# Kernel tuning notes

Measured on AMD Instinct MI355X. Metric: run time of the kernel, lower is better.

## Reference

```python
import jax, jax.numpy as jnp
import numpy as np

L, B, T, C, H, FC = 8, 4, 2048, 1024, 16, 4
HD = C // H  # head dim = 64
DFF = FC * C  # 4096


def _layernorm(x, g, b, eps=1e-5):
    mu = jnp.mean(x, axis=-1, keepdims=True)
    var = jnp.mean(jnp.square(x - mu), axis=-1, keepdims=True)
    return (x - mu) * jax.lax.rsqrt(var + eps) * g + b


def setup_inputs() -> dict:
    key = jax.random.key(0)
    ks = jax.random.split(key, 18)
    s = 0.02
    d = {}
    d["x"] = jax.random.normal(ks[0], (B, T, C), jnp.float32)
    d["ln1_g"] = jnp.ones((L, C), jnp.float32)
    d["ln1_b"] = jnp.zeros((L, C), jnp.float32)
    d["ln2_g"] = jnp.ones((L, C), jnp.float32)
    d["ln2_b"] = jnp.zeros((L, C), jnp.float32)
    d["wq"] = jax.random.normal(ks[1], (L, C, C), jnp.float32) * s
    d["bq"] = jnp.zeros((L, C), jnp.float32)
    d["wk"] = jax.random.normal(ks[2], (L, C, C), jnp.float32) * s
    d["bk"] = jnp.zeros((L, C), jnp.float32)
    d["wv"] = jax.random.normal(ks[3], (L, C, C), jnp.float32) * s
    d["bv"] = jnp.zeros((L, C), jnp.float32)
    d["wo"] = jax.random.normal(ks[4], (L, C, C), jnp.float32) * s
    d["bo"] = jnp.zeros((L, C), jnp.float32)
    d["w1"] = jax.random.normal(ks[5], (L, C, DFF), jnp.float32) * s
    d["b1"] = jnp.zeros((L, DFF), jnp.float32)
    d["w2"] = jax.random.normal(ks[6], (L, DFF, C), jnp.float32) * s
    d["b2"] = jnp.zeros((L, C), jnp.float32)
    return d


def _forward(x, ln1_g, ln1_b, ln2_g, ln2_b, wq, bq, wk, bk, wv, bv, wo, bo, w1, b1, w2, b2):
    mask = jnp.tril(jnp.ones((T, T), dtype=bool))  # causal mask (block_size buffer)
    scale = 1.0 / np.sqrt(HD).astype(np.float32)

    def block(h, p):
        g1, be1, g2, be2, Wq, Bq, Wk, Bk, Wv, Bv, Wo, Bo, W1, B1, W2, B2 = p
        hn = _layernorm(h, g1, be1)
        # heads: [B, H, T, HD]
        q = (hn @ Wq + Bq).reshape(B, T, H, HD).transpose(0, 2, 1, 3)
        k = (hn @ Wk + Bk).reshape(B, T, H, HD).transpose(0, 2, 1, 3)
        v = (hn @ Wv + Bv).reshape(B, T, H, HD).transpose(0, 2, 1, 3)
        att = jnp.einsum('bhid,bhjd->bhij', q, k) * scale
        att = jnp.where(mask, att, -jnp.inf)
        att = jax.nn.softmax(att, axis=-1)
        y = jnp.einsum('bhij,bhjd->bhid', att, v)
        y = y.transpose(0, 2, 1, 3).reshape(B, T, C) @ Wo + Bo
        h = h + y
        m = _layernorm(h, g2, be2)
        h = h + jax.nn.gelu(m @ W1 + B1, approximate=False) @ W2 + B2
        return h, None

    params = (ln1_g, ln1_b, ln2_g, ln2_b, wq, bq, wk, bk, wv, bv, wo, bo, w1, b1, w2, b2)
    x, _ = jax.lax.scan(block, x, params)
    return x


def reference(x, ln1_g, ln1_b, ln2_g, ln2_b, wq, bq, wk, bk, wv, bv, wo, bo, w1, b1, w2, b2):
    return _forward(x, ln1_g, ln1_b, ln2_g, ln2_b, wq, bq, wk, bk, wv, bv, wo, bo, w1, b1, w2, b2)
```

## Files before the change

### kernel.cpp

```cpp
#include <hip/hip_runtime.h>
#include <hip/hip_bf16.h>

#define LL 8
#define BBx 4
#define TT 2048
#define CC 1024
#define HH 16
#define HDD 64
#define DFFx 4096
#define MMx 8192

typedef __bf16 bf16;
typedef __attribute__((ext_vector_type(8))) __bf16 bf16x8;
typedef __attribute__((ext_vector_type(4))) __bf16 bf16x4;
typedef __attribute__((ext_vector_type(4))) float f32x4;
typedef __attribute__((ext_vector_type(8))) unsigned short u16x8;

#define QSCALE 0.18033688f

__device__ __forceinline__ unsigned short bfbits(float v) {
  return __builtin_bit_cast(unsigned short, (__bf16)v);
}

__device__ __forceinline__ float fexp2(float x) {
#if __has_builtin(__builtin_amdgcn_exp2f)
  return __builtin_amdgcn_exp2f(x);
#else
  float r;
  asm volatile("v_exp_f32 %0, %1\n\ts_nop 0" : "=v"(r) : "v"(x));
  return r;
#endif
}

__device__ __forceinline__ int xcd_swz(int id, int nwg) {
  return (id & 7) * (nwg >> 3) + (id >> 3);
}

#define GLDS(gp, lp) __builtin_amdgcn_global_load_lds( \
    (const __attribute__((address_space(1))) void*)(gp), \
    (__attribute__((address_space(3))) void*)(lp), 16, 0, 0)

__global__ __launch_bounds__(256) void transpose_cast(
    const float* __restrict__ W, bf16* __restrict__ Wt,
    int K, int N, long srcStride, long dstStride)
{
  __shared__ float tile[32][33];
  const float* Wl = W + (size_t)blockIdx.z * srcStride;
  bf16* Wtl = Wt + (size_t)blockIdx.z * dstStride;
  const int n0 = blockIdx.x * 32, k0 = blockIdx.y * 32;
  const int tx = threadIdx.x, ty = threadIdx.y;
#pragma unroll
  for (int i = 0; i < 32; i += 8)
    tile[ty + i][tx] = Wl[(size_t)(k0 + ty + i) * N + n0 + tx];
  __syncthreads();
#pragma unroll
  for (int i = 0; i < 32; i += 8)
    Wtl[(size_t)(n0 + ty + i) * K + k0 + tx] = (bf16)tile[tx][ty + i];
}

__global__ __launch_bounds__(256) void ln_cmb(
    float* __restrict__ h, const float* __restrict__ p0, const float* __restrict__ p1,
    const float* __restrict__ gamma, const float* __restrict__ beta,
    bf16* __restrict__ out)
{
  const int row = blockIdx.x, tid = threadIdx.x;
  const size_t base = (size_t)row * CC + tid * 4;
  float4 v = *(const float4*)(h + base);
  if (p0) {
    const float4 a = *(const float4*)(p0 + base);
    const float4 b = *(const float4*)(p1 + base);
    v.x += a.x + b.x; v.y += a.y + b.y; v.z += a.z + b.z; v.w += a.w + b.w;
    *(float4*)(h + base) = v;
  }
  if (!out) return;
  float s  = v.x + v.y + v.z + v.w;
  float ss = v.x * v.x + v.y * v.y + v.z * v.z + v.w * v.w;
#pragma unroll
  for (int o = 32; o >= 1; o >>= 1) {
    s  += __shfl_xor(s, o);
    ss += __shfl_xor(ss, o);
  }
  __shared__ float rs[4], rss[4];
  const int w = tid >> 6, l = tid & 63;
  if (l == 0) { rs[w] = s; rss[w] = ss; }
  __syncthreads();
  s  = rs[0] + rs[1] + rs[2] + rs[3];
  ss = rss[0] + rss[1] + rss[2] + rss[3];
  const float mu = s * (1.f / CC);
  const float rstd = rsqrtf(ss * (1.f / CC) - mu * mu + 1e-5f);
  const float4 g  = *(const float4*)(gamma + tid * 4);
  const float4 be = *(const float4*)(beta + tid * 4);
  bf16x4 o4;
  o4[0] = (bf16)((v.x - mu) * rstd * g.x + be.x);
  o4[1] = (bf16)((v.y - mu) * rstd * g.y + be.y);
  o4[2] = (bf16)((v.z - mu) * rstd * g.z + be.z);
  o4[3] = (bf16)((v.w - mu) * rstd * g.w + be.w);
  *(bf16x4*)(out + (size_t)row * CC + tid * 4) = o4;
}

template<int EPI>
__global__ __launch_bounds__(256, 4) void gemm128(
    const bf16* __restrict__ A, const bf16* __restrict__ Bt,
    const float* __restrict__ bias0,
    float* __restrict__ p0, float* __restrict__ p1,
    int M, int N, int K, int lda)
{
  __shared__ __align__(16) bf16 sA[128 * 64];
  __shared__ __align__(16) bf16 sB[128 * 64];
  const int nx = N >> 7;
  int wk = xcd_swz((int)blockIdx.x, (int)gridDim.x);
  int koff = 0;
  float* part = p0;
  bool addb = true;
  if constexpr (EPI == 1) {
    const int tiles = nx * (M >> 7);
    const int ks = wk / tiles;
    wk -= ks * tiles;
    koff = ks * K;
    addb = (ks == 0);
    part = ks ? p1 : p0;
  }
  const int m0 = (wk / nx) * 128;
  const int n0 = (wk % nx) * 128;
  const int tid = threadIdx.x;
  const int w = tid >> 6, l = tid & 63;
  const int wr = w >> 1, wc = w & 1;
  const int lr = l & 15, lk = l >> 4;

  f32x4 acc[4][4] = {};
  const int NT = K >> 6;

  for (int kt = 0; kt < NT; ++kt) {
#pragma unroll
    for (int i = 0; i < 4; ++i) {
      const int e = (tid << 4) + (i << 12);
      const int ro = e >> 7, co = (e & 127) >> 1;
      GLDS(A + (size_t)(m0 + ro) * lda + kt * 64 + koff + co, sA + (e >> 1));
      GLDS(Bt + (size_t)(n0 + ro) * lda + kt * 64 + koff + co, sB + (e >> 1));
    }
    __syncthreads();
#pragma unroll
    for (int kk = 0; kk < 2; ++kk) {
      bf16x8 af[4], bfr[4];
#pragma unroll
      for (int i = 0; i < 4; ++i)
        af[i] = *(const bf16x8*)&sA[(wr * 64 + i * 16 + lr) * 64 + kk * 32 + lk * 8];
#pragma unroll
      for (int j = 0; j < 4; ++j)
        bfr[j] = *(const bf16x8*)&sB[(wc * 64 + j * 16 + lr) * 64 + kk * 32 + lk * 8];
#pragma unroll
      for (int i = 0; i < 4; ++i)
#pragma unroll
        for (int j = 0; j < 4; ++j)
          acc[i][j] = __builtin_amdgcn_mfma_f32_16x16x32_bf16(af[i], bfr[j], acc[i][j], 0, 0, 0);
    }
    __syncthreads();
  }
  float bv4[4];
#pragma unroll
  for (int j = 0; j < 4; ++j)
    bv4[j] = addb ? bias0[n0 + wc * 64 + j * 16 + lr] : 0.f;
#pragma unroll
  for (int i = 0; i < 4; ++i) {
    const int mrow = m0 + wr * 64 + i * 16 + lk * 4;
#pragma unroll
    for (int r = 0; r < 4; ++r) {
      float* rowp = part + (size_t)(mrow + r) * N + n0 + wc * 64;
#pragma unroll
      for (int j = 0; j < 4; ++j)
        rowp[j * 16 + lr] = acc[i][j][r] + bv4[j];
    }
  }
  (void)M;
}

template<int EPI>
__global__ __launch_bounds__(512, 2) void gemm256(
    const bf16* __restrict__ A, const bf16* __restrict__ Bt,
    const float* __restrict__ bias0, const float* __restrict__ bias1,
    const float* __restrict__ bias2,
    bf16* __restrict__ o0, bf16* __restrict__ o1, bf16* __restrict__ o2,
    float* __restrict__ p0w, float* __restrict__ p1w,
    int M, int N, int K, int lda)
{
  __shared__ __align__(16) bf16 sA[2][256 * 64];
  __shared__ __align__(16) bf16 sB[2][256 * 64];
  const int nx = N >> 8;
  int wk = xcd_swz((int)blockIdx.x, (int)gridDim.x);
  int koff = 0;
  float* part = p0w;
  bool addb = true;
  if constexpr (EPI == 1) {
    const int tiles = nx * (M >> 8);
    const int ks = wk / tiles;
    wk -= ks * tiles;
    koff = ks * K;
    addb = (ks == 0);
    part = ks ? p1w : p0w;
  }
  const int m0 = (wk / nx) * 256;
  const int n0 = (wk % nx) * 256;
  const int tid = threadIdx.x;
  const int w = tid >> 6, l = tid & 63;
  const int wm = w >> 2, wn = w & 3;
  const int lr = l & 15, lk = l >> 4;
  const int sr = tid >> 3, ss = tid & 7;
  const int gcs = (ss ^ (sr & 7)) << 3;

  f32x4 acc[8][4] = {};
  const int NT = K >> 6;

  auto stageq = [&](int b, int kt, int q) {
    const int gc = gcs + kt * 64 + koff;
    const int rb = (q & 1) * 128;
    if (q < 2) {
#pragma unroll
      for (int i = 0; i < 2; ++i) {
        const int r = rb + sr + i * 64;
        GLDS(A + (size_t)(m0 + r) * lda + gc, &sA[b][r * 64 + ss * 8]);
      }
    } else {
#pragma unroll
      for (int i = 0; i < 2; ++i) {
        const int r = rb + sr + i * 64;
        GLDS(Bt + (size_t)(n0 + r) * lda + gc, &sB[b][r * 64 + ss * 8]);
      }
    }
  };

  stageq(0, 0, 0); stageq(0, 0, 1); stageq(0, 0, 2); stageq(0, 0, 3);
  asm volatile("s_waitcnt vmcnt(2)" ::: "memory");
  __builtin_amdgcn_s_barrier();

  bf16x8 af[8], bf2[2];
  for (int t = 0; t < NT; ++t) {
    const int cur = t & 1, nxt = cur ^ 1;
    const bool pre = (t + 1 < NT);
#pragma unroll
    for (int ph = 0; ph < 4; ++ph) {
      const int kk = ph >> 1, nh = ph & 1;
      if (nh == 0) {
#pragma unroll
        for (int m = 0; m < 8; ++m) {
          const int row = wm * 128 + m * 16 + lr;
          af[m] = *(const bf16x8*)&sA[cur][row * 64 + (((kk * 4 + lk) ^ (row & 7)) << 3)];
        }
      }
#pragma unroll
      for (int j2 = 0; j2 < 2; ++j2) {
        const int row = nh * 128 + wn * 32 + j2 * 16 + lr;
        bf2[j2] = *(const bf16x8*)&sB[cur][row * 64 + (((kk * 4 + lk) ^ (row & 7)) << 3)];
      }
      if (pre) stageq(nxt, t + 1, ph);
      if (ph == 0 || ph == 3) {
        if (pre) asm volatile("s_waitcnt vmcnt(2)" ::: "memory");
        else     asm volatile("s_waitcnt vmcnt(0)" ::: "memory");
      }
      __builtin_amdgcn_s_barrier();
      asm volatile("s_waitcnt lgkmcnt(0)" ::: "memory");
      __builtin_amdgcn_sched_barrier(0);
      __builtin_amdgcn_s_setprio(1);
#pragma unroll
      for (int m = 0; m < 8; ++m)
#pragma unroll
        for (int j2 = 0; j2 < 2; ++j2)
          acc[m][nh * 2 + j2] = __builtin_amdgcn_mfma_f32_16x16x32_bf16(
              af[m], bf2[j2], acc[m][nh * 2 + j2], 0, 0, 0);
      __builtin_amdgcn_s_setprio(0);
      __builtin_amdgcn_s_barrier();
    }
  }

  if constexpr (EPI == 0) {
    const int seg = n0 >> 10;
    const float* bp = (seg == 0) ? bias0 : (seg == 1 ? bias1 : bias2);
    if (seg < 2) {
      const float qs = (seg == 0) ? QSCALE : 1.0f;
      float bv4[4];
      int hh4[4], dd4[4];
#pragma unroll
      for (int jj = 0; jj < 4; ++jj) {
        const int c1024 = (n0 + (jj >> 1) * 128 + wn * 32 + (jj & 1) * 16 + lr) & 1023;
        bv4[jj] = bp[c1024];
        hh4[jj] = c1024 >> 6;
        dd4[jj] = c1024 & 63;
      }
      bf16* dst = (seg == 0) ? o0 : o1;
#pragma unroll
      for (int m = 0; m < 8; ++m) {
        const int mrow = m0 + wm * 128 + m * 16 + lk * 4;
        const int bidx = mrow >> 11, t = mrow & 2047;
#pragma unroll
        for (int r = 0; r < 4; ++r) {
#pragma unroll
          for (int jj = 0; jj < 4; ++jj)
            dst[(((size_t)(bidx * HH + hh4[jj])) * TT + t + r) * HDD + dd4[jj]] =
                (bf16)((acc[m][jj][r] + bv4[jj]) * qs);
        }
      }
    } else {
      char* scb = (char*)((w < 4) ? (&sA[0][0] + w * 8192) : (&sB[0][0] + (w - 4) * 8192));
#pragma unroll
      for (int jj = 0; jj < 4; ++jj) {
        const int dloc = (jj >> 1) * 32 + (jj & 1) * 16 + lr;
        const int dglob = (n0 & 1023) + (jj >> 1) * 128 + wn * 32 + (jj & 1) * 16 + lr;
        const float bv = bias2[dglob];
#pragma unroll
        for (int m = 0; m < 8; ++m) {
          ushort4 pk;
          pk.x = bfbits(acc[m][jj][0] + bv);
          pk.y = bfbits(acc[m][jj][1] + bv);
          pk.z = bfbits(acc[m][jj][2] + bv);
          pk.w = bfbits(acc[m][jj][3] + bv);
          *(ushort4*)(scb + dloc * 256 + (((m * 16 + lk * 4) * 2) ^ ((dloc & 7) << 4))) = pk;
        }
      }
      asm volatile("s_waitcnt lgkmcnt(0)" ::: "memory");
      const int bidx = m0 >> 11;
      const int tb = (m0 & 2047) + wm * 128;
      const int c = l & 15;
#pragma unroll
      for (int g = 0; g < 16; ++g) {
        const int dloc = g * 4 + lk;
        const int dglob = (n0 & 1023) + (dloc >> 5) * 128 + wn * 32 + (dloc & 31);
        const int hh = dglob >> 6, dd = dglob & 63;
        u16x8 val = *(const u16x8*)(scb + dloc * 256 + ((c * 16) ^ ((dloc & 7) << 4)));
        *(u16x8*)&o2[(((size_t)(bidx * HH + hh)) * HDD + dd) * TT + tb + c * 8] = val;
      }
    }
  } else if constexpr (EPI == 1) {
    float bv4[4];
#pragma unroll
    for (int jj = 0; jj < 4; ++jj)
      bv4[jj] = addb ? bias0[n0 + (jj >> 1) * 128 + wn * 32 + (jj & 1) * 16 + lr] : 0.f;
#pragma unroll
    for (int m = 0; m < 8; ++m) {
      const int mrow = m0 + wm * 128 + m * 16 + lk * 4;
#pragma unroll
      for (int r = 0; r < 4; ++r) {
        float* rowp = part + (size_t)(mrow + r) * N + n0 + wn * 32;
        rowp[lr]        = acc[m][0][r] + bv4[0];
        rowp[16 + lr]   = acc[m][1][r] + bv4[1];
        rowp[128 + lr]  = acc[m][2][r] + bv4[2];
        rowp[144 + lr]  = acc[m][3][r] + bv4[3];
      }
    }
  } else {
    float bv4[4];
#pragma unroll
    for (int jj = 0; jj < 4; ++jj)
      bv4[jj] = bias0[n0 + (jj >> 1) * 128 + wn * 32 + (jj & 1) * 16 + lr];
#pragma unroll
    for (int m = 0; m < 8; ++m) {
      const int mrow = m0 + wm * 128 + m * 16 + lk * 4;
#pragma unroll
      for (int r = 0; r < 4; ++r) {
        bf16* rowp = o0 + (size_t)(mrow + r) * N + n0 + wn * 32;
        const float x0 = acc[m][0][r] + bv4[0];
        const float x1 = acc[m][1][r] + bv4[1];
        const float x2 = acc[m][2][r] + bv4[2];
        const float x3 = acc[m][3][r] + bv4[3];
        rowp[lr]       = (bf16)(0.5f * x0 * (1.f + erff(x0 * 0.70710678f)));
        rowp[16 + lr]  = (bf16)(0.5f * x1 * (1.f + erff(x1 * 0.70710678f)));
        rowp[128 + lr] = (bf16)(0.5f * x2 * (1.f + erff(x2 * 0.70710678f)));
        rowp[144 + lr] = (bf16)(0.5f * x3 * (1.f + erff(x3 * 0.70710678f)));
      }
    }
  }
  (void)M;
}

__global__ __launch_bounds__(256) void attn_fwd(
    const bf16* __restrict__ Q, const bf16* __restrict__ Kk,
    const bf16* __restrict__ Vt, bf16* __restrict__ O)
{
  const int wk = xcd_swz((int)blockIdx.x, (int)gridDim.x);
  const int bh = wk >> 3;
  const int xt = wk & 7;
  const int tid = threadIdx.x;
  const int w = tid >> 6, l = tid & 63;
  const int lr = l & 15, lk = l >> 4;
  const int bidx = bh >> 4, hh = bh & 15;

  const bf16* Qp = Q  + (size_t)bh * (TT * HDD);
  const bf16* Kp = Kk + (size_t)bh * (TT * HDD);
  const bf16* Vp = Vt + (size_t)bh * (HDD * TT);

  __shared__ __align__(16) bf16 sK[64 * 64];
  __shared__ __align__(16) bf16 sV[64 * 64];
  __shared__ __align__(16) bf16 sP[4][16 * 64];
  bf16* sPw = &sP[w][0];

  const int swz = (lr & 7) * 8;
  const int srow = tid >> 3;
  const int scol = (((tid & 7) ^ (srow & 7)) << 3);
  const int sdst = tid << 3;

  for (int half = 0; half < 2; ++half) {
    const int qtile = (half == 0) ? xt : (15 - xt);
    const int q0 = qtile * 128;

    bf16x8 qf[2][2];
#pragma unroll
    for (int qi = 0; qi < 2; ++qi)
#pragma unroll
      for (int dk = 0; dk < 2; ++dk)
        qf[qi][dk] = *(const bf16x8*)&Qp[(size_t)(q0 + w * 32 + qi * 16 + lr) * HDD + dk * 32 + lk * 8];

    f32x4 accO[2][4] = {};
    float mrun[2] = {-__builtin_inff(), -__builtin_inff()};
    float lrun[2] = {0.f, 0.f};
    const int wqmax = q0 + w * 32 + 31;
    const int kvend = q0 + 128;

    for (int kv = 0; kv < kvend; kv += 64) {
      __syncthreads();
#pragma unroll
      for (int i = 0; i < 2; ++i) {
        GLDS(Kp + (size_t)(kv + srow + i * 32) * HDD + scol, sK + sdst + i * 2048);
        GLDS(Vp + (size_t)(srow + i * 32) * TT + kv + scol, sV + sdst + i * 2048);
      }
      __syncthreads();

      if (kv <= wqmax) {
#pragma unroll
        for (int qi = 0; qi < 2; ++qi) {
          f32x4 st[4];
#pragma unroll
          for (int kt = 0; kt < 4; ++kt) {
            f32x4 z = {0.f, 0.f, 0.f, 0.f};
#pragma unroll
            for (int dk = 0; dk < 2; ++dk) {
              bf16x8 kf = *(const bf16x8*)&sK[(kt * 16 + lr) * 64 + ((dk * 32 + lk * 8) ^ swz)];
              z = __builtin_amdgcn_mfma_f32_16x16x32_bf16(kf, qf[qi][dk], z, 0, 0, 0);
            }
            st[kt] = z;
          }
          const int qabs_base = q0 + w * 32 + qi * 16;
          float pm = -__builtin_inff();
          if (kv + 63 > qabs_base) {
            const int qabs = qabs_base + lr;
#pragma unroll
            for (int kt = 0; kt < 4; ++kt)
#pragma unroll
              for (int r = 0; r < 4; ++r) {
                const int kvabs = kv + kt * 16 + lk * 4 + r;
                float val = (kvabs > qabs) ? -__builtin_inff() : st[kt][r];
                st[kt][r] = val;
                pm = fmaxf(pm, val);
              }
          } else {
#pragma unroll
            for (int kt = 0; kt < 4; ++kt)
#pragma unroll
              for (int r = 0; r < 4; ++r) pm = fmaxf(pm, st[kt][r]);
          }
          pm = fmaxf(pm, __shfl_xor(pm, 16));
          pm = fmaxf(pm, __shfl_xor(pm, 32));
          const float mnew = fmaxf(mrun[qi], pm);
          const float alpha = fexp2(mrun[qi] - mnew);
          mrun[qi] = mnew;
          float psum = 0.f;
#pragma unroll
          for (int kt = 0; kt < 4; ++kt) {
            const float p0v = fexp2(st[kt][0] - mnew);
            const float p1v = fexp2(st[kt][1] - mnew);
            const float p2v = fexp2(st[kt][2] - mnew);
            const float p3v = fexp2(st[kt][3] - mnew);
            psum += p0v + p1v + p2v + p3v;
            ushort4 pk;
            pk.x = bfbits(p0v); pk.y = bfbits(p1v); pk.z = bfbits(p2v); pk.w = bfbits(p3v);
            *(ushort4*)&sPw[lr * 64 + ((kt * 16 + lk * 4) ^ swz)] = pk;
          }
          psum += __shfl_xor(psum, 16);
          psum += __shfl_xor(psum, 32);
          lrun[qi] = lrun[qi] * alpha + psum;
          f32x4 al4;
#pragma unroll
          for (int r = 0; r < 4; ++r) al4[r] = __shfl(alpha, lk * 4 + r);
#pragma unroll
          for (int dj = 0; dj < 4; ++dj) accO[qi][dj] *= al4;
#pragma unroll
          for (int kt2 = 0; kt2 < 2; ++kt2) {
            bf16x8 pf = *(const bf16x8*)&sPw[lr * 64 + ((kt2 * 32 + lk * 8) ^ swz)];
#pragma unroll
            for (int dj = 0; dj < 4; ++dj) {
              bf16x8 vf = *(const bf16x8*)&sV[(dj * 16 + lr) * 64 + ((kt2 * 32 + lk * 8) ^ swz)];
              accO[qi][dj] = __builtin_amdgcn_mfma_f32_16x16x32_bf16(pf, vf, accO[qi][dj], 0, 0, 0);
            }
          }
        }
      }
    }

#pragma unroll
    for (int qi = 0; qi < 2; ++qi) {
      const float linv = 1.f / lrun[qi];
      f32x4 li4;
#pragma unroll
      for (int r = 0; r < 4; ++r) li4[r] = __shfl(linv, lk * 4 + r);
      const int tbase = q0 + w * 32 + qi * 16 + lk * 4;
#pragma unroll
      for (int dj = 0; dj < 4; ++dj)
#pragma unroll
        for (int r = 0; r < 4; ++r)
          O[((size_t)bidx * TT + tbase + r) * CC + hh * 64 + dj * 16 + lr] =
              (bf16)(accO[qi][dj][r] * li4[r]);
    }
  }
}

extern "C" void kernel_launch(void* const* d_in, const int* in_sizes, int n_in,
                              void* d_out, int out_size, void* d_ws, size_t ws_size,
                              hipStream_t stream)
{
  const float* x    = (const float*)d_in[0];
  const float* ln1g = (const float*)d_in[1];
  const float* ln1b = (const float*)d_in[2];
  const float* ln2g = (const float*)d_in[3];
  const float* ln2b = (const float*)d_in[4];
  const float* wq   = (const float*)d_in[5];
  const float* bq   = (const float*)d_in[6];
  const float* wk   = (const float*)d_in[7];
  const float* bk   = (const float*)d_in[8];
  const float* wv   = (const float*)d_in[9];
  const float* bvv  = (const float*)d_in[10];
  const float* wo   = (const float*)d_in[11];
  const float* bo   = (const float*)d_in[12];
  const float* w1   = (const float*)d_in[13];
  const float* b1   = (const float*)d_in[14];
  const float* w2   = (const float*)d_in[15];
  const float* b2   = (const float*)d_in[16];

  float* h = (float*)d_out;
  bf16* ws = (bf16*)d_ws;
  bf16* wqkvT = ws;
  bf16* woT   = wqkvT + (size_t)LL * 3 * CC * CC;
  bf16* w1T   = woT + (size_t)LL * CC * CC;
  bf16* w2T   = w1T + (size_t)LL * CC * DFFx;
  bf16* hn    = w2T + (size_t)LL * CC * DFFx;
  bf16* qb    = hn + (size_t)MMx * CC;
  bf16* kb    = qb + (size_t)MMx * CC;
  bf16* vt    = kb + (size_t)MMx * CC;
  bf16* ab    = vt + (size_t)MMx * CC;
  bf16* mid   = ab + (size_t)MMx * CC;

  float* pw0 = (float*)mid;
  float* pw1 = (float*)mid + (size_t)MMx * CC;
  float* pm0 = (float*)qb;
  float* pm1 = (float*)vt;

  hipMemcpyAsync(h, x, (size_t)MMx * CC * sizeof(float), hipMemcpyDeviceToDevice, stream);

  dim3 tb(32, 8);
  transpose_cast<<<dim3(CC / 32, CC / 32, LL), tb, 0, stream>>>(wq, wqkvT, CC, CC, (long)CC * CC, (long)3 * CC * CC);
  transpose_cast<<<dim3(CC / 32, CC / 32, LL), tb, 0, stream>>>(wk, wqkvT + CC * CC, CC, CC, (long)CC * CC, (long)3 * CC * CC);
  transpose_cast<<<dim3(CC / 32, CC / 32, LL), tb, 0, stream>>>(wv, wqkvT + 2 * CC * CC, CC, CC, (long)CC * CC, (long)3 * CC * CC);
  transpose_cast<<<dim3(CC / 32, CC / 32, LL), tb, 0, stream>>>(wo, woT, CC, CC, (long)CC * CC, (long)CC * CC);
  transpose_cast<<<dim3(DFFx / 32, CC / 32, LL), tb, 0, stream>>>(w1, w1T, CC, DFFx, (long)CC * DFFx, (long)CC * DFFx);
  transpose_cast<<<dim3(CC / 32, DFFx / 32, LL), tb, 0, stream>>>(w2, w2T, DFFx, CC, (long)CC * DFFx, (long)CC * DFFx);

  for (int li = 0; li < LL; ++li) {
    if (li == 0)
      ln_cmb<<<MMx, 256, 0, stream>>>(h, nullptr, nullptr, ln1g, ln1b, hn);
    else
      ln_cmb<<<MMx, 256, 0, stream>>>(h, pm0, pm1, ln1g + li * CC, ln1b + li * CC, hn);
    gemm256<0><<<(3 * CC / 256) * (MMx / 256), 512, 0, stream>>>(
        hn, wqkvT + (size_t)li * 3 * CC * CC, bq + li * CC, bk + li * CC, bvv + li * CC,
        qb, kb, vt, nullptr, nullptr, MMx, 3 * CC, CC, CC);
    attn_fwd<<<8 * BBx * HH, 256, 0, stream>>>(qb, kb, vt, ab);
    gemm128<1><<<2 * (CC / 128) * (MMx / 128), 256, 0, stream>>>(
        ab, woT + (size_t)li * CC * CC, bo + li * CC, pw0, pw1, MMx, CC, CC / 2, CC);
    ln_cmb<<<MMx, 256, 0, stream>>>(h, pw0, pw1, ln2g + li * CC, ln2b + li * CC, hn);
    gemm256<2><<<(DFFx / 256) * (MMx / 256), 512, 0, stream>>>(
        hn, w1T + (size_t)li * CC * DFFx, b1 + li * DFFx, nullptr, nullptr,
        mid, nullptr, nullptr, nullptr, nullptr, MMx, DFFx, CC, CC);
    gemm256<1><<<2 * (CC / 256) * (MMx / 256), 512, 0, stream>>>(
        mid, w2T + (size_t)li * CC * DFFx, b2 + li * CC, nullptr, nullptr,
        nullptr, nullptr, nullptr, pm0, pm1, MMx, CC, DFFx / 2, DFFx);
  }
  ln_cmb<<<MMx, 256, 0, stream>>>(h, pm0, pm1, nullptr, nullptr, nullptr);
  (void)in_sizes; (void)n_in; (void)out_size; (void)ws_size;
}
```

Measured before the change: 3.315 ms.

## Restructure GEMM mainloop into 8-phase quadrant schedule with finer-grained LDS prefetch

The bf16 GEMM mainloop now processes two K-tiles per iteration in eight phases. Each phase computes one 128x128 quadrant of the 256x256 tile over both k-halves, instead of four phases that reload all A fragments. Global-to-LDS staging is split into half-tiles issued at staggered phases, and the next tile's A/B halves are prefetched earlier, with vmcnt waits moved after the MFMA block. The aim is better overlap of global loads with MFMA work and fewer live A-fragment registers. In exchange it adds more barriers and more complex wait counting, which risks hazards on the shared double buffer.

```diff
diff --git a/kernel.cpp b/kernel.cpp
--- a/kernel.cpp
+++ b/kernel.cpp
@@ -210,16 +210,19 @@
   f32x4 acc[8][4] = {};
   const int NT = K >> 6;
 
-  auto stageq = [&](int b, int kt, int q) {
+  auto stageh = [&](int kt, int q) {
+    if (kt >= NT) return;
+    const int b = kt & 1;
     const int gc = gcs + kt * 64 + koff;
-    const int rb = (q & 1) * 128;
     if (q < 2) {
+      const int hq = q & 1;
 #pragma unroll
       for (int i = 0; i < 2; ++i) {
-        const int r = rb + sr + i * 64;
+        const int r = i * 128 + hq * 64 + sr;
         GLDS(A + (size_t)(m0 + r) * lda + gc, &sA[b][r * 64 + ss * 8]);
       }
     } else {
+      const int rb = (q & 1) * 128;
 #pragma unroll
       for (int i = 0; i < 2; ++i) {
         const int r = rb + sr + i * 64;
@@ -228,45 +231,57 @@
     }
   };
 
-  stageq(0, 0, 0); stageq(0, 0, 1); stageq(0, 0, 2); stageq(0, 0, 3);
-  asm volatile("s_waitcnt vmcnt(2)" ::: "memory");
+  stageh(0, 0); stageh(0, 1); stageh(0, 2); stageh(0, 3);
+  stageh(1, 0); stageh(1, 2);
+  asm volatile("s_waitcnt vmcnt(4)" ::: "memory");
   __builtin_amdgcn_s_barrier();
 
-  bf16x8 af[8], bf2[2];
-  for (int t = 0; t < NT; ++t) {
-    const int cur = t & 1, nxt = cur ^ 1;
-    const bool pre = (t + 1 < NT);
-#pragma unroll
-    for (int ph = 0; ph < 4; ++ph) {
-      const int kk = ph >> 1, nh = ph & 1;
-      if (nh == 0) {
-#pragma unroll
-        for (int m = 0; m < 8; ++m) {
-          const int row = wm * 128 + m * 16 + lr;
-          af[m] = *(const bf16x8*)&sA[cur][row * 64 + (((kk * 4 + lk) ^ (row & 7)) << 3)];
-        }
-      }
-#pragma unroll
-      for (int j2 = 0; j2 < 2; ++j2) {
-        const int row = nh * 128 + wn * 32 + j2 * 16 + lr;
-        bf2[j2] = *(const bf16x8*)&sB[cur][row * 64 + (((kk * 4 + lk) ^ (row & 7)) << 3)];
-      }
-      if (pre) stageq(nxt, t + 1, ph);
-      if (ph == 0 || ph == 3) {
-        if (pre) asm volatile("s_waitcnt vmcnt(2)" ::: "memory");
-        else     asm volatile("s_waitcnt vmcnt(0)" ::: "memory");
-      }
+  for (int t = 0; t < NT; t += 2) {
+#pragma unroll
+    for (int ph = 0; ph < 8; ++ph) {
+      const int kt = t + (ph >> 2);
+      const int cur = kt & 1;
+      const int mh = (ph >> 1) & 1, nh = ph & 1;
+      bf16x8 af[4][2], bfv[2][2];
+#pragma unroll
+      for (int mi = 0; mi < 4; ++mi) {
+        const int row = wm * 128 + mh * 64 + mi * 16 + lr;
+#pragma unroll
+        for (int kk = 0; kk < 2; ++kk)
+          af[mi][kk] = *(const bf16x8*)&sA[cur][row * 64 + (((kk * 4 + lk) ^ (row & 7)) << 3)];
+      }
+#pragma unroll
+      for (int jj = 0; jj < 2; ++jj) {
+        const int row = nh * 128 + wn * 32 + jj * 16 + lr;
+#pragma unroll
+        for (int kk = 0; kk < 2; ++kk)
+          bfv[jj][kk] = *(const bf16x8*)&sB[cur][row * 64 + (((kk * 4 + lk) ^ (row & 7)) << 3)];
+      }
+      if      (ph == 0) stageh(t + 1, 1);
+      else if (ph == 1) stageh(t + 1, 3);
+      else if (ph == 2) stageh(t + 2, 0);
+      else if (ph == 3) stageh(t + 2, 2);
+      else if (ph == 4) stageh(t + 2, 1);
+      else if (ph == 5) stageh(t + 2, 3);
+      else if (ph == 6) stageh(t + 3, 0);
+      else              stageh(t + 3, 2);
       __builtin_amdgcn_s_barrier();
       asm volatile("s_waitcnt lgkmcnt(0)" ::: "memory");
       __builtin_amdgcn_sched_barrier(0);
       __builtin_amdgcn_s_setprio(1);
 #pragma unroll
-      for (int m = 0; m < 8; ++m)
-#pragma unroll
-        for (int j2 = 0; j2 < 2; ++j2)
-          acc[m][nh * 2 + j2] = __builtin_amdgcn_mfma_f32_16x16x32_bf16(
-              af[m], bf2[j2], acc[m][nh * 2 + j2], 0, 0, 0);
+      for (int mi = 0; mi < 4; ++mi)
+#pragma unroll
+        for (int jj = 0; jj < 2; ++jj)
+#pragma unroll
+          for (int kk = 0; kk < 2; ++kk)
+            acc[mh * 4 + mi][nh * 2 + jj] = __builtin_amdgcn_mfma_f32_16x16x32_bf16(
+                af[mi][kk], bfv[jj][kk], acc[mh * 4 + mi][nh * 2 + jj], 0, 0, 0);
       __builtin_amdgcn_s_setprio(0);
+      if (ph == 3 || ph == 7) {
+        if (t + 2 < NT) asm volatile("s_waitcnt vmcnt(4)" ::: "memory");
+        else            asm volatile("s_waitcnt vmcnt(0)" ::: "memory");
+      }
       __builtin_amdgcn_s_barrier();
     }
   }
```

After: 3.421 ms. 3.2% more time.
